# Optimization experiments

Hardware: AMD Instinct MI355X
Metric: run time of the kernel (lower is better)

Reference implementation:

```python
import jax, jax.numpy as jnp
import numpy as np

B = 32        # number of groups (batch.unique())
L = 512       # max_len (equal-size groups in this setup)
E = 512       # embed_dim
H = 8         # num_heads
N = B * L


def setup_inputs() -> dict:
    key = jax.random.key(0)
    k1, k2, k3 = jax.random.split(key, 3)
    embeddings = jax.random.normal(k1, (N, E), dtype=jnp.float32)
    # sorted group ids; equal group sizes keep max_len static for jit
    batch = jnp.repeat(jnp.arange(B, dtype=jnp.int32), L)
    in_proj_w = jax.random.normal(k2, (3 * E, E), dtype=jnp.float32) * (1.0 / np.sqrt(E))
    in_proj_b = jnp.zeros((3 * E,), dtype=jnp.float32)
    out_proj_w = jax.random.normal(k3, (E, E), dtype=jnp.float32) * (1.0 / np.sqrt(E))
    out_proj_b = jnp.zeros((E,), dtype=jnp.float32)
    return {"embeddings": embeddings, "batch": batch,
            "in_proj_w": in_proj_w, "in_proj_b": in_proj_b,
            "out_proj_w": out_proj_w, "out_proj_b": out_proj_b}


def reference(embeddings, batch, in_proj_w, in_proj_b, out_proj_w, out_proj_b):
    Dh = E // H
    ones = jnp.ones_like(batch, dtype=jnp.int32)
    counts = jax.ops.segment_sum(ones, batch, num_segments=B)          # [B]
    starts = jnp.cumsum(counts) - counts                               # exclusive cumsum
    pos = jnp.arange(N, dtype=jnp.int32) - starts[batch]               # position within group
    # pad ragged -> [B, L, E] (zeros for padding, as in torch code)
    padded = jnp.zeros((B, L, E), dtype=embeddings.dtype).at[batch, pos].set(embeddings)
    # FAITHFUL float attn_mask: +1.0 added to scores outside the valid block
    valid = (jnp.arange(L)[None, :] < counts[:, None]).astype(embeddings.dtype)  # [B, L]
    add_mask = 1.0 - valid[:, :, None] * valid[:, None, :]             # [B, Lq, Lk]

    qkv = padded @ in_proj_w.T + in_proj_b                             # [B, L, 3E]
    q, k, v = jnp.split(qkv, 3, axis=-1)
    q = q.reshape(B, L, H, Dh)
    k = k.reshape(B, L, H, Dh)
    v = v.reshape(B, L, H, Dh)
    scale = 1.0 / np.sqrt(Dh)
    scores = jnp.einsum('bqhd,bkhd->bhqk', q, k) * scale + add_mask[:, None, :, :]
    attn = jax.nn.softmax(scores, axis=-1)
    ctx = jnp.einsum('bhqk,bkhd->bqhd', attn, v).reshape(B, L, E)
    attn_out = ctx @ out_proj_w.T + out_proj_b                         # [B, L, E]
    # max_pool1d over sequence (includes padded query rows, as original)
    return jnp.max(attn_out, axis=1)                                   # [B, E]
```

## Files before the change

### kernel.cpp

```cpp
#include <hip/hip_runtime.h>
#include <math.h>


#define B_ 32
#define L_ 512
#define E_ 512
#define H_ 8
#define DH 64
#define N_ (B_ * L_)
#define EMB_N (N_ * E_)
#define IPW_N (3 * E_ * E_)
#define OPW_N (E_ * E_)

typedef _Float16 f16;
typedef __attribute__((ext_vector_type(8))) _Float16 f16x8;
typedef __attribute__((ext_vector_type(4))) float f32x4;
typedef unsigned short u16;

__device__ __forceinline__ u16 f16_bits(float x) {
    f16 h = (f16)x;
    return *reinterpret_cast<u16*>(&h);
}
__device__ __forceinline__ unsigned pk2(float a, float b) {
    return (unsigned)f16_bits(a) | ((unsigned)f16_bits(b) << 16);
}
__device__ __forceinline__ unsigned pkrtz(float a, float b) {
    auto r = __builtin_amdgcn_cvt_pkrtz(a, b);
    return *reinterpret_cast<unsigned*>(&r);
}
__device__ __forceinline__ void async16(const void* g, void* l) {
    __builtin_amdgcn_global_load_lds(
        (const __attribute__((address_space(1))) void*)g,
        (__attribute__((address_space(3))) void*)l, 16, 0, 0);
}

__device__ __forceinline__ void atomicMaxFloat(float* addr, float val) {
    if (val >= 0.0f) atomicMax((int*)addr, __float_as_int(val));
    else             atomicMin((unsigned int*)addr, __float_as_uint(val));
}

__global__ __launch_bounds__(256) void cvt_kernel(
        const float* __restrict__ emb, const float* __restrict__ ipw,
        const float* __restrict__ opw,
        u16* __restrict__ eh, u16* __restrict__ wh, u16* __restrict__ oh,
        float* __restrict__ out) {
    if (blockIdx.x < 16) {
        int o = blockIdx.x * 1024 + threadIdx.x * 4;
        float4 ninf = make_float4(-INFINITY, -INFINITY, -INFINITY, -INFINITY);
        *(float4*)(out + o) = ninf;
    }
    size_t i = ((size_t)blockIdx.x * 256 + threadIdx.x) * 8;
    const float* src; u16* dst; size_t off;
    if (i < EMB_N)              { src = emb; dst = eh; off = i; }
    else if (i < EMB_N + IPW_N) { src = ipw; dst = wh; off = i - EMB_N; }
    else                        { src = opw; dst = oh; off = i - EMB_N - IPW_N; }
    float4 a = *(const float4*)(src + off);
    float4 b = *(const float4*)(src + off + 4);
    uint4 p;
    p.x = pk2(a.x, a.y); p.y = pk2(a.z, a.w);
    p.z = pk2(b.x, b.y); p.w = pk2(b.z, b.w);
    *(uint4*)(dst + off) = p;
}

__global__ __launch_bounds__(512) void qkv_mfma(
        const u16* __restrict__ Wg, const u16* __restrict__ Eg,
        const float* __restrict__ bias,
        u16* __restrict__ qg, u16* __restrict__ kg, u16* __restrict__ vg) {
    __shared__ u16 Ah[2][128 * 32];
    __shared__ u16 Bh[2][256 * 32];
    const int tok0 = blockIdx.x * 256, row0 = blockIdx.y * 128;
    const int tid = threadIdx.x, wave = tid >> 6, lane = tid & 63;
    const int quad = lane >> 4, c = lane & 15;
    const int ww = wave & 1, wt = wave >> 1;
    const int sw = (quad ^ ((c >> 1) & 3)) * 8;
    const bool vblk = (row0 >= 1024);

    f32x4 zero = {0.f, 0.f, 0.f, 0.f};
    f32x4 acc[4][4];
#pragma unroll
    for (int i = 0; i < 4; i++)
#pragma unroll
        for (int j = 0; j < 4; j++) acc[i][j] = zero;

    auto stage = [&](int buf, int kt) {
        {
            int chunk = wave * 64 + lane;
            int r = chunk >> 2, g = chunk & 3;
            int pos = g ^ ((r >> 1) & 3);
            async16(Wg + (size_t)(row0 + r) * E_ + kt * 32 + pos * 8,
                    &Ah[buf][wave * 512]);
        }
#pragma unroll
        for (int it = 0; it < 2; it++) {
            int chunk = (it * 8 + wave) * 64 + lane;
            int r = chunk >> 2, g = chunk & 3;
            int pos = g ^ ((r >> 1) & 3);
            async16(Eg + (size_t)(tok0 + r) * E_ + kt * 32 + pos * 8,
                    &Bh[buf][(it * 8 + wave) * 512]);
        }
    };

    stage(0, 0);
    for (int kt = 0; kt < 16; kt++) {
        __syncthreads();
        if (kt < 15) stage((kt + 1) & 1, kt + 1);
        const int buf = kt & 1;
        f16x8 mf[4], nf[4];
        if (!vblk) {
#pragma unroll
            for (int i = 0; i < 4; i++)
                mf[i] = *(const f16x8*)&Ah[buf][(ww * 64 + i * 16 + c) * 32 + sw];
#pragma unroll
            for (int j = 0; j < 4; j++)
                nf[j] = *(const f16x8*)&Bh[buf][(wt * 64 + j * 16 + c) * 32 + sw];
        } else {
#pragma unroll
            for (int i = 0; i < 4; i++)
                mf[i] = *(const f16x8*)&Bh[buf][(wt * 64 + i * 16 + c) * 32 + sw];
#pragma unroll
            for (int j = 0; j < 4; j++)
                nf[j] = *(const f16x8*)&Ah[buf][(ww * 64 + j * 16 + c) * 32 + sw];
        }
#pragma unroll
        for (int i = 0; i < 4; i++)
#pragma unroll
            for (int j = 0; j < 4; j++)
                acc[i][j] = __builtin_amdgcn_mfma_f32_16x16x32_f16(mf[i], nf[j], acc[i][j], 0, 0, 0);
    }

    if (!vblk) {
        const int which = row0 >> 9;
        u16* dst = which ? kg : qg;
        const float scale = which ? 1.0f : 0.18033688f;
        const int h = (((row0 & 511) + ww * 64) >> 6);
#pragma unroll
        for (int i = 0; i < 4; i++) {
            const int d0 = i * 16 + quad * 4;
            float4 bv = *(const float4*)(bias + row0 + ww * 64 + d0);
            const int dch = i * 2 + (quad >> 1);
#pragma unroll
            for (int j = 0; j < 4; j++) {
                int n = tok0 + wt * 64 + j * 16 + c;
                int bb = n >> 9, l = n & 511;
                uint2 st;
                st.x = pk2((acc[i][j][0] + bv.x) * scale, (acc[i][j][1] + bv.y) * scale);
                st.y = pk2((acc[i][j][2] + bv.z) * scale, (acc[i][j][3] + bv.w) * scale);
                size_t addr = (size_t)(bb * H_ + h) * 32768 +
                              (l >> 4) * 1024 + dch * 128 + (l & 15) * 8 + (quad & 1) * 4;
                *(uint2*)(dst + addr) = st;
            }
        }
    } else {
        const int bb = tok0 >> 9;
        const int l0 = (tok0 & 511) + wt * 64;
        const int tt = l0 >> 6;
        const int h = (((row0 & 511) + ww * 64) >> 6);
#pragma unroll
        for (int j = 0; j < 4; j++) {
            int mw = row0 + ww * 64 + j * 16 + c;
            float bv = bias[mw];
#pragma unroll
            for (int ip = 0; ip < 2; ip++) {
                uint4 st;
                st.x = pk2(acc[2 * ip][j][0] + bv, acc[2 * ip][j][1] + bv);
                st.y = pk2(acc[2 * ip][j][2] + bv, acc[2 * ip][j][3] + bv);
                st.z = pk2(acc[2 * ip + 1][j][0] + bv, acc[2 * ip + 1][j][1] + bv);
                st.w = pk2(acc[2 * ip + 1][j][2] + bv, acc[2 * ip + 1][j][3] + bv);
                size_t addr = (size_t)(bb * H_ + h) * 32768 + tt * 4096 +
                              j * 1024 + ip * 512 + quad * 128 + c * 8;
                *(uint4*)(vg + addr) = st;
            }
        }
    }
}

__global__ __launch_bounds__(256, 2) void attn_mfma(
        const u16* __restrict__ qg, const u16* __restrict__ kg,
        const u16* __restrict__ vg, u16* __restrict__ ctx) {
    const int qt = blockIdx.x, h = blockIdx.y, b = blockIdx.z;
    const int tid = threadIdx.x, wave = tid >> 6, lane = tid & 63;
    const int quad = lane >> 4, c = lane & 15;
    const size_t base = (size_t)(b * H_ + h) * 32768;
    const int lane8 = lane * 8;

    f16x8 qf[4][2];
#pragma unroll
    for (int rs = 0; rs < 4; rs++) {
        const size_t qb = base + (size_t)(qt * 16 + wave * 4 + rs) * 1024;
#pragma unroll
        for (int kk = 0; kk < 2; kk++)
            qf[rs][kk] = *(const f16x8*)(qg + qb + kk * 512 + lane8);
    }

    f32x4 zero = {0.f, 0.f, 0.f, 0.f};
    const f32x4 m6 = {-6.f, -6.f, -6.f, -6.f};
    f16x8 ones;
#pragma unroll
    for (int i = 0; i < 8; i++) ones[i] = (f16)1.0f;

    f32x4 Of[4][4];
    f32x4 lacc[4];
#pragma unroll
    for (int rs = 0; rs < 4; rs++) {
        lacc[rs] = zero;
#pragma unroll
        for (int j = 0; j < 4; j++) Of[rs][j] = zero;
    }

#pragma unroll
    for (int kt = 0; kt < 8; kt++) {
        const size_t tb = base + (size_t)kt * 4096;
        f16x8 kf[4][2];
#pragma unroll
        for (int jj = 0; jj < 4; jj++)
#pragma unroll
            for (int kk = 0; kk < 2; kk++)
                kf[jj][kk] = *(const f16x8*)(kg + tb + jj * 1024 + kk * 512 + lane8);
        f16x8 vf[2][4];
#pragma unroll
        for (int kk = 0; kk < 2; kk++)
#pragma unroll
            for (int j = 0; j < 4; j++)
                vf[kk][j] = *(const f16x8*)(vg + tb + j * 1024 + kk * 512 + lane8);

#pragma unroll
        for (int rs = 0; rs < 4; rs++) {
            f32x4 Sf[4];
            __builtin_amdgcn_s_setprio(1);
#pragma unroll
            for (int jj = 0; jj < 4; jj++) {
                Sf[jj] = m6;
#pragma unroll
                for (int kk = 0; kk < 2; kk++)
                    Sf[jj] = __builtin_amdgcn_mfma_f32_16x16x32_f16(kf[jj][kk], qf[rs][kk], Sf[jj], 0, 0, 0);
            }
            __builtin_amdgcn_s_setprio(0);
            unsigned w[8];
#pragma unroll
            for (int jj = 0; jj < 4; jj++) {
                w[2 * jj]     = pkrtz(exp2f(Sf[jj][0]), exp2f(Sf[jj][1]));
                w[2 * jj + 1] = pkrtz(exp2f(Sf[jj][2]), exp2f(Sf[jj][3]));
            }
            union { uint4 u; f16x8 v; } u0, u1;
            u0.u = make_uint4(w[0], w[1], w[2], w[3]);
            u1.u = make_uint4(w[4], w[5], w[6], w[7]);
            f16x8 pf0 = u0.v, pf1 = u1.v;
            __builtin_amdgcn_s_setprio(1);
            lacc[rs] = __builtin_amdgcn_mfma_f32_16x16x32_f16(ones, pf0, lacc[rs], 0, 0, 0);
            lacc[rs] = __builtin_amdgcn_mfma_f32_16x16x32_f16(ones, pf1, lacc[rs], 0, 0, 0);
#pragma unroll
            for (int j = 0; j < 4; j++) {
                Of[rs][j] = __builtin_amdgcn_mfma_f32_16x16x32_f16(vf[0][j], pf0, Of[rs][j], 0, 0, 0);
                Of[rs][j] = __builtin_amdgcn_mfma_f32_16x16x32_f16(vf[1][j], pf1, Of[rs][j], 0, 0, 0);
            }
            __builtin_amdgcn_s_setprio(0);
        }
    }

#pragma unroll
    for (int rs = 0; rs < 4; rs++) {
        float inv = 1.0f / lacc[rs][0];
        int n = b * L_ + qt * 256 + wave * 64 + rs * 16 + c;
#pragma unroll
        for (int j = 0; j < 4; j++) {
            int d0 = j * 16 + quad * 4;
            uint2 st;
            st.x = pk2(Of[rs][j][0] * inv, Of[rs][j][1] * inv);
            st.y = pk2(Of[rs][j][2] * inv, Of[rs][j][3] * inv);
            *(uint2*)(ctx + (size_t)n * E_ + h * DH + d0) = st;
        }
    }
}

__global__ __launch_bounds__(256) void proj_mfma(
        const u16* __restrict__ Ag, const u16* __restrict__ Bg,
        const float* __restrict__ bias, float* __restrict__ out) {
    __shared__ u16 Ah[2][128 * 32], Bh[2][128 * 32];
    __shared__ float red[2][128];
    const int row0 = blockIdx.x * 128, col0 = blockIdx.y * 128;
    const int tid = threadIdx.x, wave = tid >> 6, lane = tid & 63;
    const int quad = lane >> 4, c = lane & 15;
    const int wr = (wave >> 1) * 64, wc = (wave & 1) * 64;
    const int sw = (quad ^ ((c >> 1) & 3)) * 8;

    f32x4 zero = {0.f, 0.f, 0.f, 0.f};
    f32x4 acc[4][4];
#pragma unroll
    for (int i = 0; i < 4; i++)
#pragma unroll
        for (int j = 0; j < 4; j++) acc[i][j] = zero;

    auto stage = [&](int buf, int kt) {
#pragma unroll
        for (int it = 0; it < 2; it++) {
            int chunk = (wave * 2 + it) * 64 + lane;
            int r = chunk >> 2, g = chunk & 3;
            int pos = g ^ ((r >> 1) & 3);
            int lbase = (wave * 2 + it) * 512;
            async16(Ag + (size_t)(row0 + r) * E_ + kt * 32 + pos * 8, &Ah[buf][lbase]);
            async16(Bg + (size_t)(col0 + r) * E_ + kt * 32 + pos * 8, &Bh[buf][lbase]);
        }
    };

    stage(0, 0);
    for (int kt = 0; kt < 16; kt++) {
        __syncthreads();
        if (kt < 15) stage((kt + 1) & 1, kt + 1);
        const int buf = kt & 1;
        f16x8 af[4], bf[4];
#pragma unroll
        for (int i = 0; i < 4; i++)
            af[i] = *(const f16x8*)&Ah[buf][(wr + i * 16 + c) * 32 + sw];
#pragma unroll
        for (int j = 0; j < 4; j++)
            bf[j] = *(const f16x8*)&Bh[buf][(wc + j * 16 + c) * 32 + sw];
#pragma unroll
        for (int i = 0; i < 4; i++)
#pragma unroll
            for (int j = 0; j < 4; j++)
                acc[i][j] = __builtin_amdgcn_mfma_f32_16x16x32_f16(af[i], bf[j], acc[i][j], 0, 0, 0);
    }

    float cm[4];
#pragma unroll
    for (int j = 0; j < 4; j++) {
        cm[j] = -INFINITY;
#pragma unroll
        for (int i = 0; i < 4; i++)
#pragma unroll
            for (int r = 0; r < 4; r++) cm[j] = fmaxf(cm[j], acc[i][j][r]);
        cm[j] = fmaxf(cm[j], __shfl_xor(cm[j], 16));
        cm[j] = fmaxf(cm[j], __shfl_xor(cm[j], 32));
    }
    if (quad == 0)
#pragma unroll
        for (int j = 0; j < 4; j++) red[wave >> 1][wc + j * 16 + c] = cm[j];
    __syncthreads();
    if (tid < 128) {
        int bb = row0 >> 9;
        float m = fmaxf(red[0][tid], red[1][tid]) + bias[col0 + tid];
        atomicMaxFloat(&out[(size_t)bb * E_ + col0 + tid], m);
    }
}

extern "C" void kernel_launch(void* const* d_in, const int* in_sizes, int n_in,
                              void* d_out, int out_size, void* d_ws, size_t ws_size,
                              hipStream_t stream) {
    const float* emb = (const float*)d_in[0];
    const float* ipw = (const float*)d_in[2];
    const float* ipb = (const float*)d_in[3];
    const float* opw = (const float*)d_in[4];
    const float* opb = (const float*)d_in[5];
    float* out = (float*)d_out;

    u16* eh  = (u16*)d_ws;
    u16* wh  = eh + EMB_N;
    u16* oh  = wh + IPW_N;
    u16* qg  = oh + OPW_N;
    u16* kg  = qg + (size_t)N_ * E_;
    u16* vg  = kg + (size_t)N_ * E_;
    u16* ctx = vg + (size_t)N_ * E_;

    cvt_kernel<<<(EMB_N + IPW_N + OPW_N) / (256 * 8), 256, 0, stream>>>(
        emb, ipw, opw, eh, wh, oh, out);
    qkv_mfma<<<dim3(N_ / 256, (3 * E_) / 128), 512, 0, stream>>>(
        wh, eh, ipb, qg, kg, vg);
    attn_mfma<<<dim3(L_ / 256, H_, B_), 256, 0, stream>>>(qg, kg, vg, ctx);
    proj_mfma<<<dim3(N_ / 128, E_ / 128), 256, 0, stream>>>(ctx, oh, opb, out);
}
```

Baseline: 156.6 us.

## Load QKV weight fragments directly from global and triple-buffer token tiles

The weight operand of the QKV projection GEMM is now read straight from global memory into registers, skipping the LDS round trip. The token tile stays in LDS but moves to a three-stage ring with explicit vmcnt waits and one raw barrier per step, replacing the __syncthreads double buffer. The aim is to cut LDS traffic and barrier stalls and to prefetch deeper. In exchange, each wave issues uncached direct global loads for the weights (reuse now relies on L2/L1), and the vmcnt counts must match the number of async loads issued per stage.

```diff
diff --git a/kernel.cpp b/kernel.cpp
--- a/kernel.cpp
+++ b/kernel.cpp
@@ -66,8 +66,7 @@
         const u16* __restrict__ Wg, const u16* __restrict__ Eg,
         const float* __restrict__ bias,
         u16* __restrict__ qg, u16* __restrict__ kg, u16* __restrict__ vg) {
-    __shared__ u16 Ah[2][128 * 32];
-    __shared__ u16 Bh[2][256 * 32];
+    __shared__ u16 Bh[3][256 * 32];
     const int tok0 = blockIdx.x * 256, row0 = blockIdx.y * 128;
     const int tid = threadIdx.x, wave = tid >> 6, lane = tid & 63;
     const int quad = lane >> 4, c = lane & 15;
@@ -83,13 +82,6 @@
         for (int j = 0; j < 4; j++) acc[i][j] = zero;
 
     auto stage = [&](int buf, int kt) {
-        {
-            int chunk = wave * 64 + lane;
-            int r = chunk >> 2, g = chunk & 3;
-            int pos = g ^ ((r >> 1) & 3);
-            async16(Wg + (size_t)(row0 + r) * E_ + kt * 32 + pos * 8,
-                    &Ah[buf][wave * 512]);
-        }
 #pragma unroll
         for (int it = 0; it < 2; it++) {
             int chunk = (it * 8 + wave) * 64 + lane;
@@ -100,26 +92,38 @@
         }
     };
 
+    const int wrow = row0 + ww * 64;
+
     stage(0, 0);
+    stage(1, 1);
     for (int kt = 0; kt < 16; kt++) {
-        __syncthreads();
-        if (kt < 15) stage((kt + 1) & 1, kt + 1);
-        const int buf = kt & 1;
+        if (kt < 15) asm volatile("s_waitcnt vmcnt(2)" ::: "memory");
+        else         asm volatile("s_waitcnt vmcnt(0)" ::: "memory");
+        __builtin_amdgcn_s_barrier();
+        __builtin_amdgcn_sched_barrier(0);
+
+        f16x8 wf[4];
+        const int ko = kt * 32 + quad * 8;
+#pragma unroll
+        for (int i = 0; i < 4; i++)
+            wf[i] = *(const f16x8*)(Wg + (size_t)(wrow + i * 16 + c) * E_ + ko);
+
+        if (kt < 14) stage((kt + 2) % 3, kt + 2);
+
+        const u16* Bb = &Bh[kt % 3][0];
         f16x8 mf[4], nf[4];
         if (!vblk) {
 #pragma unroll
+            for (int i = 0; i < 4; i++) mf[i] = wf[i];
+#pragma unroll
+            for (int j = 0; j < 4; j++)
+                nf[j] = *(const f16x8*)&Bb[(wt * 64 + j * 16 + c) * 32 + sw];
+        } else {
+#pragma unroll
             for (int i = 0; i < 4; i++)
-                mf[i] = *(const f16x8*)&Ah[buf][(ww * 64 + i * 16 + c) * 32 + sw];
-#pragma unroll
-            for (int j = 0; j < 4; j++)
-                nf[j] = *(const f16x8*)&Bh[buf][(wt * 64 + j * 16 + c) * 32 + sw];
-        } else {
-#pragma unroll
-            for (int i = 0; i < 4; i++)
-                mf[i] = *(const f16x8*)&Bh[buf][(wt * 64 + i * 16 + c) * 32 + sw];
-#pragma unroll
-            for (int j = 0; j < 4; j++)
-                nf[j] = *(const f16x8*)&Ah[buf][(ww * 64 + j * 16 + c) * 32 + sw];
+                mf[i] = *(const f16x8*)&Bb[(wt * 64 + i * 16 + c) * 32 + sw];
+#pragma unroll
+            for (int j = 0; j < 4; j++) nf[j] = wf[j];
         }
 #pragma unroll
         for (int i = 0; i < 4; i++)
```

Result: slower. 198.8 us (+26.9%).
